# Optimization experiments

Hardware: AMD Instinct MI355X
Metric: run time of the kernel (lower is better)

The kernel has to match this reference:

```python
import jax, jax.numpy as jnp
import numpy as np

KEEP_RATIO = 0.25
BLOCK = 8
TEMP = 0.1


def setup_inputs() -> dict:
    key = jax.random.key(0)
    features = jax.random.normal(key, (8, 256, 132, 132), dtype=jnp.float32)
    return {"features": features, "enabled": 1}


def reference(features, enabled):
    B, C, H, W = features.shape
    if not enabled:
        return jnp.ones((B, C, H, W), dtype=features.dtype)
    # pad H, W up to multiples of BLOCK (zeros, like F.pad default)
    ph = (-H) % BLOCK
    pw = (-W) % BLOCK
    x = jnp.pad(jnp.abs(features), ((0, 0), (0, 0), (0, ph), (0, pw)))
    Hp, Wp = H + ph, W + pw
    nh, nw = Hp // BLOCK, Wp // BLOCK
    # avg_pool2d(kernel=stride=BLOCK) == block-mean via reshape
    pooled = x.reshape(B, C, nh, BLOCK, nw, BLOCK).mean(axis=(3, 5))  # [B,C,nh,nw]
    total = nh * nw
    scores = pooled.reshape(B, C, total)
    keep = max(1, min(total, int(round(total * KEEP_RATIO))))
    top_vals, top_idx = jax.lax.top_k(scores, keep)  # sorted descending, like torch.topk
    # hard mask: scatter ones at topk indices
    flat_idx = top_idx.reshape(B * C, keep)
    hard = (jnp.zeros((B * C, total), dtype=features.dtype)
            .at[jnp.arange(B * C)[:, None], flat_idx].set(1.0)
            .reshape(B, C, total))
    # training-mode straight-through soft blend
    thr = jax.lax.stop_gradient(top_vals[..., -1:])  # kth value as threshold
    soft = jax.nn.sigmoid((scores - thr) / TEMP)
    soft = soft * (keep / jnp.maximum(soft.sum(-1, keepdims=True), 1e-6))
    soft = jnp.clip(soft, 0.0, 1.0)
    mask = jax.lax.stop_gradient(hard) - jax.lax.stop_gradient(soft) + soft
    # upsample blocks back to pixels (repeat_interleave) and crop padding
    block_mask = mask.reshape(B, C, nh, nw)
    full = jnp.repeat(jnp.repeat(block_mask, BLOCK, axis=2), BLOCK, axis=3)
    return full[:, :, :H, :W]
```

## Files before the change

### kernel.cpp

```cpp
#include <hip/hip_runtime.h>


#define HH 132
#define WW 132
#define NB 17
#define TOTAL 289
#define NPAD 320
#define KEEP 72
#define NTH 256
#define NC4 33
#define NV 4356
#define PLANES 2048

typedef float floatx4 __attribute__((ext_vector_type(4)));

__global__ __launch_bounds__(NTH)
void gate_kernel(const float4* __restrict__ feats4,
                 const int* __restrict__ enabled_p,
                 float4* __restrict__ out4) {
    const int plane = blockIdx.x;
    const int t = threadIdx.x;
    const float4* __restrict__ fp = feats4 + (size_t)plane * NV;

    __shared__ __align__(16) float    s_e[NV];
    __shared__ __align__(16) unsigned s_key[NPAD];
    __shared__ float s_hard[TOTAL];
    __shared__ unsigned s_T;
    __shared__ int s_kT;

    #pragma unroll
    for (int k = 0; k < 18; ++k) {
        const int v = t + k * NTH;
        if (v < NV) {
            const float4 x = fp[v];
            s_e[v] = (fabsf(x.x) + fabsf(x.y)) + (fabsf(x.z) + fabsf(x.w));
        }
    }
    __syncthreads();

    for (int b = t; b < NPAD; b += NTH) {
        unsigned key = 0u;
        if (b < TOTAL) {
            const int br = b / NB;
            const int bc = b - br * NB;
            const int nr = (br == NB - 1) ? 4 : 8;
            const int base = (br * 8) * NC4 + 2 * bc;
            double sum = 0.0;
            if (bc < NB - 1) {
                for (int rr = 0; rr < nr; ++rr)
                    sum += (double)s_e[base + rr * NC4]
                         + (double)s_e[base + rr * NC4 + 1];
            } else {
                for (int rr = 0; rr < nr; ++rr)
                    sum += (double)s_e[base + rr * NC4];
            }
            key = __float_as_uint((float)sum);
        }
        s_key[b] = key;
    }
    __syncthreads();

    if (t < 64) {
        unsigned K0 = s_key[t];
        unsigned K1 = s_key[64 + t];
        unsigned K2 = s_key[128 + t];
        unsigned K3 = s_key[192 + t];
        unsigned K4 = s_key[256 + t];
        unsigned P = 0u;
        int k = KEEP;
        #pragma unroll
        for (int b = 31; b >= 0; --b) {
            const unsigned hi = (P >> b) | 1u;
            int cnt = __popcll(__ballot((K0 >> b) == hi))
                    + __popcll(__ballot((K1 >> b) == hi))
                    + __popcll(__ballot((K2 >> b) == hi))
                    + __popcll(__ballot((K3 >> b) == hi))
                    + __popcll(__ballot((K4 >> b) == hi));
            if (cnt >= k) P |= (1u << b);
            else          k -= cnt;
        }
        if (t == 0) { s_T = P; s_kT = k; }
    }
    __syncthreads();

    const int en = *enabled_p;
    const unsigned T = s_T;
    const int kT = s_kT;
    for (int i = t; i < TOTAL; i += NTH) {
        const unsigned ki = s_key[i];
        float m;
        if (!en || ki > T) {
            m = 1.0f;
        } else if (ki < T) {
            m = 0.0f;
        } else {
            int eq = 0;
            for (int j = 0; j < i; ++j) eq += (int)(s_key[j] == T);
            m = (eq < kT) ? 1.0f : 0.0f;
        }
        s_hard[i] = m;
    }
    __syncthreads();

    floatx4* __restrict__ op = (floatx4*)(out4 + (size_t)plane * NV);
    for (int v = t; v < NV; v += NTH) {
        const int base = v * 4;
        const int row = base / WW;
        const int col = base - row * WW;
        const float m = s_hard[(row >> 3) * NB + (col >> 3)];
        const floatx4 mv = {m, m, m, m};
        __builtin_nontemporal_store(mv, &op[v]);
    }
}

extern "C" void kernel_launch(void* const* d_in, const int* in_sizes, int n_in,
                              void* d_out, int out_size, void* d_ws, size_t ws_size,
                              hipStream_t stream) {
    const float4* feats = (const float4*)d_in[0];
    const int* enabled = (const int*)d_in[1];
    float4* out = (float4*)d_out;
    gate_kernel<<<PLANES, NTH, 0, stream>>>(feats, enabled, out);
}
```

Measured before the change: 260.8 us.

## Split abs-sum into a grid-stride pre-pass kernel writing to workspace

Splits the single per-plane kernel in two. A grid-stride kernel first computes the abs-sum of each float4 into a workspace buffer, and a second per-plane kernel then reads those sums and does the block pooling, radix top-k and mask write. The aim is to read the large input at full occupancy, separate from the shared-memory-heavy selection stage. The cost is an extra write and read of an intermediate buffer a quarter the size of the input, plus a second launch. The original fused kernel is kept as a fallback when the workspace is missing or too small.

```diff
diff --git a/kernel.cpp b/kernel.cpp
--- a/kernel.cpp
+++ b/kernel.cpp
@@ -11,16 +11,27 @@
 #define NC4 33
 #define NV 4356
 #define PLANES 2048
+#define NTOT (PLANES * NV)
 
 typedef float floatx4 __attribute__((ext_vector_type(4)));
 
 __global__ __launch_bounds__(NTH)
-void gate_kernel(const float4* __restrict__ feats4,
+void sum_kernel(const float4* __restrict__ in4,
+                float* __restrict__ ws_sum) {
+    const int stride = gridDim.x * NTH;
+    for (int i = blockIdx.x * NTH + threadIdx.x; i < NTOT; i += stride) {
+        const float4 x = in4[i];
+        ws_sum[i] = (fabsf(x.x) + fabsf(x.y)) + (fabsf(x.z) + fabsf(x.w));
+    }
+}
+
+__global__ __launch_bounds__(NTH)
+void mask_kernel(const float* __restrict__ ws_sum,
                  const int* __restrict__ enabled_p,
                  float4* __restrict__ out4) {
     const int plane = blockIdx.x;
     const int t = threadIdx.x;
-    const float4* __restrict__ fp = feats4 + (size_t)plane * NV;
+    const float* __restrict__ sp = ws_sum + (size_t)plane * NV;
 
     __shared__ __align__(16) float    s_e[NV];
     __shared__ __align__(16) unsigned s_key[NPAD];
@@ -31,10 +42,7 @@
     #pragma unroll
     for (int k = 0; k < 18; ++k) {
         const int v = t + k * NTH;
-        if (v < NV) {
-            const float4 x = fp[v];
-            s_e[v] = (fabsf(x.x) + fabsf(x.y)) + (fabsf(x.z) + fabsf(x.w));
-        }
+        if (v < NV) s_e[v] = sp[v];
     }
     __syncthreads();
 
@@ -113,11 +121,111 @@
     }
 }
 
+__global__ __launch_bounds__(NTH)
+void gate_mono(const float4* __restrict__ feats4,
+               const int* __restrict__ enabled_p,
+               float4* __restrict__ out4) {
+    const int plane = blockIdx.x;
+    const int t = threadIdx.x;
+    const float4* __restrict__ fp = feats4 + (size_t)plane * NV;
+
+    __shared__ __align__(16) float    s_e[NV];
+    __shared__ __align__(16) unsigned s_key[NPAD];
+    __shared__ float s_hard[TOTAL];
+    __shared__ unsigned s_T;
+    __shared__ int s_kT;
+
+    #pragma unroll
+    for (int k = 0; k < 18; ++k) {
+        const int v = t + k * NTH;
+        if (v < NV) {
+            const float4 x = fp[v];
+            s_e[v] = (fabsf(x.x) + fabsf(x.y)) + (fabsf(x.z) + fabsf(x.w));
+        }
+    }
+    __syncthreads();
+    for (int b = t; b < NPAD; b += NTH) {
+        unsigned key = 0u;
+        if (b < TOTAL) {
+            const int br = b / NB;
+            const int bc = b - br * NB;
+            const int nr = (br == NB - 1) ? 4 : 8;
+            const int base = (br * 8) * NC4 + 2 * bc;
+            double sum = 0.0;
+            if (bc < NB - 1) {
+                for (int rr = 0; rr < nr; ++rr)
+                    sum += (double)s_e[base + rr * NC4]
+                         + (double)s_e[base + rr * NC4 + 1];
+            } else {
+                for (int rr = 0; rr < nr; ++rr)
+                    sum += (double)s_e[base + rr * NC4];
+            }
+            key = __float_as_uint((float)sum);
+        }
+        s_key[b] = key;
+    }
+    __syncthreads();
+    if (t < 64) {
+        unsigned K0 = s_key[t];
+        unsigned K1 = s_key[64 + t];
+        unsigned K2 = s_key[128 + t];
+        unsigned K3 = s_key[192 + t];
+        unsigned K4 = s_key[256 + t];
+        unsigned P = 0u;
+        int k = KEEP;
+        #pragma unroll
+        for (int b = 31; b >= 0; --b) {
+            const unsigned hi = (P >> b) | 1u;
+            int cnt = __popcll(__ballot((K0 >> b) == hi))
+                    + __popcll(__ballot((K1 >> b) == hi))
+                    + __popcll(__ballot((K2 >> b) == hi))
+                    + __popcll(__ballot((K3 >> b) == hi))
+                    + __popcll(__ballot((K4 >> b) == hi));
+            if (cnt >= k) P |= (1u << b);
+            else          k -= cnt;
+        }
+        if (t == 0) { s_T = P; s_kT = k; }
+    }
+    __syncthreads();
+    const int en = *enabled_p;
+    const unsigned T = s_T;
+    const int kT = s_kT;
+    for (int i = t; i < TOTAL; i += NTH) {
+        const unsigned ki = s_key[i];
+        float m;
+        if (!en || ki > T)      m = 1.0f;
+        else if (ki < T)        m = 0.0f;
+        else {
+            int eq = 0;
+            for (int j = 0; j < i; ++j) eq += (int)(s_key[j] == T);
+            m = (eq < kT) ? 1.0f : 0.0f;
+        }
+        s_hard[i] = m;
+    }
+    __syncthreads();
+    floatx4* __restrict__ op = (floatx4*)(out4 + (size_t)plane * NV);
+    for (int v = t; v < NV; v += NTH) {
+        const int base = v * 4;
+        const int row = base / WW;
+        const int col = base - row * WW;
+        const float m = s_hard[(row >> 3) * NB + (col >> 3)];
+        const floatx4 mv = {m, m, m, m};
+        __builtin_nontemporal_store(mv, &op[v]);
+    }
+}
+
 extern "C" void kernel_launch(void* const* d_in, const int* in_sizes, int n_in,
                               void* d_out, int out_size, void* d_ws, size_t ws_size,
                               hipStream_t stream) {
     const float4* feats = (const float4*)d_in[0];
     const int* enabled = (const int*)d_in[1];
     float4* out = (float4*)d_out;
-    gate_kernel<<<PLANES, NTH, 0, stream>>>(feats, enabled, out);
-}
+    const size_t need = (size_t)NTOT * sizeof(float);
+    if (d_ws != nullptr && ws_size >= need) {
+        float* wsum = (float*)d_ws;
+        sum_kernel<<<4096, NTH, 0, stream>>>(feats, wsum);
+        mask_kernel<<<PLANES, NTH, 0, stream>>>(wsum, enabled, out);
+    } else {
+        gate_mono<<<PLANES, NTH, 0, stream>>>(feats, enabled, out);
+    }
+}
```

Result: no change. 265.0 us (+1.6%).
